# Kernel tuning notes

Measured on AMD Instinct MI355X. Metric: run time of the kernel, lower is better.

## Reference

```python
import jax, jax.numpy as jnp
import numpy as np

EPS = 1e-5
NEG_SLOPE = 0.01  # torch F.leaky_relu default


def _batchnorm(h, gamma, beta):
    # BatchNorm1d in training mode: batch stats over node dim, biased variance
    mu = jnp.mean(h, axis=0)
    var = jnp.mean((h - mu) ** 2, axis=0)
    return gamma * (h - mu) * jax.lax.rsqrt(var + EPS) + beta


def setup_inputs() -> dict:
    N, E, H, ED = 16384, 524288, 128, 16
    key = jax.random.key(0)
    ks = jax.random.split(key, 12)
    s = 1.0 / np.sqrt(H)
    return {
        "x": jax.random.normal(ks[0], (N, H), jnp.float32),
        "edge_index": jax.random.randint(ks[1], (2, E), 0, N, jnp.int64),
        "edge_attr": jax.random.normal(ks[2], (E, ED), jnp.float32),
        "Wq": jax.random.normal(ks[3], (H, H), jnp.float32) * s,
        "bq": jnp.zeros((H,), jnp.float32),
        "Wk": jax.random.normal(ks[4], (H, H), jnp.float32) * s,
        "bk": jnp.zeros((H,), jnp.float32),
        "Wv": jax.random.normal(ks[5], (H, H), jnp.float32) * s,
        "bv": jnp.zeros((H,), jnp.float32),
        "We": jax.random.normal(ks[6], (ED, 1), jnp.float32) * (1.0 / np.sqrt(ED)),
        "be": jnp.zeros((1,), jnp.float32),
        "bn1_g": jnp.ones((H,), jnp.float32),
        "bn1_b": jnp.zeros((H,), jnp.float32),
        "W1": jax.random.normal(ks[7], (H, 2 * H), jnp.float32) * s,
        "b1": jnp.zeros((2 * H,), jnp.float32),
        "W2": jax.random.normal(ks[8], (2 * H, H), jnp.float32) * (1.0 / np.sqrt(2 * H)),
        "b2": jnp.zeros((H,), jnp.float32),
        "bn2_g": jnp.ones((H,), jnp.float32),
        "bn2_b": jnp.zeros((H,), jnp.float32),
    }


def reference(x, edge_index, edge_attr, Wq, bq, Wk, bk, Wv, bv, We, be,
              bn1_g, bn1_b, W1, b1, W2, b2, bn2_g, bn2_b):
    N = x.shape[0]
    Q = x @ Wq + bq  # [N, H]
    K = x @ Wk + bk
    V = x @ Wv + bv
    Ebias = (edge_attr @ We + be)[:, 0]  # [E], num_heads == 1
    src, dst = edge_index[0], edge_index[1]
    # per-edge dot product over the FULL hidden dim (as in the source)
    scores = jnp.sum(Q[src] * K[dst], axis=1) + Ebias  # [E]
    scores = jnp.where(scores >= 0, scores, NEG_SLOPE * scores)
    # to_dense_adj scatter-adds edge_attr into a dense [N, N] adjacency
    adj = jnp.zeros((N, N), x.dtype).at[src, dst].add(scores)
    attn = jax.nn.softmax(adj, axis=1)  # dense softmax incl. zero non-edges
    x_new = attn @ V  # [N, H]
    h = _batchnorm(x + x_new, bn1_g, bn1_b)
    ffn = jax.nn.relu(h @ W1 + b1) @ W2 + b2
    return _batchnorm(h + ffn, bn2_g, bn2_b)
```

## Files before the change

kernel.cpp:

```cpp
#include <hip/hip_runtime.h>
#include <hip/hip_bf16.h>
#include <math.h>

#define H 128
#define H2 256
#define SLAB 96
#define LDA 136
#define LDA2 264
#define EPS 1e-5f

typedef __attribute__((ext_vector_type(8))) short s16x8;
typedef __attribute__((ext_vector_type(4))) float f32x4;

__device__ __forceinline__ unsigned short f2bf(float f) {
  unsigned u = __float_as_uint(f);
  unsigned r = (u + 0x7FFFu + ((u >> 16) & 1u)) >> 16;
  return (unsigned short)r;
}
__device__ __forceinline__ float bf2f(unsigned short s) {
  return __uint_as_float(((unsigned)s) << 16);
}

__global__ void wprep(const float* __restrict__ Wq, const float* __restrict__ Wk,
                      const float* __restrict__ Wv, const float* __restrict__ W1,
                      const float* __restrict__ W2,
                      short* qh, short* ql, short* kh, short* kl,
                      short* vh, short* w1h, short* w2h,
                      int* __restrict__ cnt, float* __restrict__ stats, int N)
{
  int job = blockIdx.z;
  if (job == 5) {
    int t = blockIdx.x * 256 + threadIdx.x;
    if (t < N) cnt[t] = 0;
    if (t < 72 * H) stats[t] = 0.f;
    return;
  }
  const float* src; short* dh; short* dl = nullptr; int Kd, Nn;
  if (job == 0)      { src = Wq; dh = qh;  dl = ql; Kd = 128; Nn = 128; }
  else if (job == 1) { src = Wk; dh = kh;  dl = kl; Kd = 128; Nn = 128; }
  else if (job == 2) { src = Wv; dh = vh;           Kd = 128; Nn = 128; }
  else if (job == 3) { src = W1; dh = w1h;          Kd = 128; Nn = 256; }
  else               { src = W2; dh = w2h;          Kd = 256; Nn = 128; }
  int t = blockIdx.x * 256 + threadIdx.x;
  if (t >= Kd * Nn) return;
  int n = t / Kd, k = t - n * Kd;
  float v = src[(size_t)k * Nn + n];
  unsigned short h = f2bf(v);
  dh[t] = (short)h;
  if (dl) dl[t] = (short)f2bf(v - bf2f(h));
}

__global__ __launch_bounds__(256) void qkv_mfma(
    const float* __restrict__ x,
    const short* __restrict__ Wqh, const short* __restrict__ Wql,
    const short* __restrict__ Wkh, const short* __restrict__ Wkl,
    const short* __restrict__ Wvh,
    const float* __restrict__ bq, const float* __restrict__ bk,
    const float* __restrict__ bv,
    float* __restrict__ Q, unsigned short* __restrict__ Kbf,
    unsigned short* __restrict__ Vbf, float* __restrict__ SVp)
{
  __shared__ __align__(16) short Ahi[64 * LDA];
  __shared__ __align__(16) short Alo[64 * LDA];
  int tid = threadIdx.x;
  int bm = blockIdx.x * 64;
  int wave = tid >> 6, lane = tid & 63;
  int quad = lane >> 4, l16 = lane & 15;
  int wn = wave * 32;

#pragma unroll
  for (int i = 0; i < 4; ++i) {
    int g = i * 256 + tid;
    int row = g >> 4, f = g & 15;
    const float4* xp = (const float4*)&x[(size_t)(bm + row) * H + f * 8];
    float4 v0 = xp[0], v1 = xp[1];
    float vv[8] = {v0.x, v0.y, v0.z, v0.w, v1.x, v1.y, v1.z, v1.w};
    s16x8 hv, lv;
#pragma unroll
    for (int j = 0; j < 8; ++j) {
      unsigned short hh = f2bf(vv[j]);
      hv[j] = (short)hh;
      lv[j] = (short)f2bf(vv[j] - bf2f(hh));
    }
    *(s16x8*)&Ahi[row * LDA + f * 8] = hv;
    *(s16x8*)&Alo[row * LDA + f * 8] = lv;
  }
  __syncthreads();

  for (int ph = 0; ph < 3; ++ph) {
    const short* Bh = (ph == 0) ? Wqh : (ph == 1) ? Wkh : Wvh;
    const short* Bl = (ph == 0) ? Wql : (ph == 1) ? Wkl : nullptr;

    s16x8 bh[2][4], bl2[2][4];
#pragma unroll
    for (int nt = 0; nt < 2; ++nt)
#pragma unroll
      for (int ks = 0; ks < 4; ++ks)
        bh[nt][ks] = *(const s16x8*)&Bh[(size_t)(wn + nt * 16 + l16) * H + ks * 32 + quad * 8];
    if (Bl) {
#pragma unroll
      for (int nt = 0; nt < 2; ++nt)
#pragma unroll
        for (int ks = 0; ks < 4; ++ks)
          bl2[nt][ks] = *(const s16x8*)&Bl[(size_t)(wn + nt * 16 + l16) * H + ks * 32 + quad * 8];
    }

    f32x4 acc[4][2];
#pragma unroll
    for (int mt = 0; mt < 4; ++mt)
#pragma unroll
      for (int nt = 0; nt < 2; ++nt) acc[mt][nt] = (f32x4){0.f, 0.f, 0.f, 0.f};

#pragma unroll
    for (int ks = 0; ks < 4; ++ks) {
      int kof = ks * 32 + quad * 8;
      s16x8 ah[4], al[4];
#pragma unroll
      for (int mt = 0; mt < 4; ++mt) {
        ah[mt] = *(s16x8*)&Ahi[(mt * 16 + l16) * LDA + kof];
        al[mt] = *(s16x8*)&Alo[(mt * 16 + l16) * LDA + kof];
      }
#pragma unroll
      for (int mt = 0; mt < 4; ++mt)
#pragma unroll
        for (int nt = 0; nt < 2; ++nt) {
          acc[mt][nt] = __builtin_amdgcn_mfma_f32_16x16x32_bf16(ah[mt], bh[nt][ks], acc[mt][nt], 0, 0, 0);
          if (ph < 2) {
            acc[mt][nt] = __builtin_amdgcn_mfma_f32_16x16x32_bf16(ah[mt], bl2[nt][ks], acc[mt][nt], 0, 0, 0);
            acc[mt][nt] = __builtin_amdgcn_mfma_f32_16x16x32_bf16(al[mt], bh[nt][ks], acc[mt][nt], 0, 0, 0);
          }
        }
    }

    if (ph == 0) {
#pragma unroll
      for (int nt = 0; nt < 2; ++nt) {
        int col = wn + nt * 16 + l16;
        float bb = bq[col];
#pragma unroll
        for (int mt = 0; mt < 4; ++mt)
#pragma unroll
          for (int r = 0; r < 4; ++r) {
            int row = bm + mt * 16 + quad * 4 + r;
            Q[(size_t)row * H + col] = acc[mt][nt][r] + bb;
          }
      }
    } else if (ph == 1) {
#pragma unroll
      for (int nt = 0; nt < 2; ++nt) {
        int col = wn + nt * 16 + l16;
        float bb = bk[col];
#pragma unroll
        for (int mt = 0; mt < 4; ++mt)
#pragma unroll
          for (int r = 0; r < 4; ++r) {
            int row = bm + mt * 16 + quad * 4 + r;
            Kbf[(size_t)row * H + col] = f2bf(acc[mt][nt][r] + bb);
          }
      }
    } else {
      int bank = blockIdx.x & 7;
#pragma unroll
      for (int nt = 0; nt < 2; ++nt) {
        int col = wn + nt * 16 + l16;
        float bb = bv[col];
        float ps = 0.f;
#pragma unroll
        for (int mt = 0; mt < 4; ++mt)
#pragma unroll
          for (int r = 0; r < 4; ++r) {
            int row = bm + mt * 16 + quad * 4 + r;
            float v = acc[mt][nt][r] + bb;
            Vbf[(size_t)row * H + col] = f2bf(v);
            ps += v;
          }
        ps += __shfl_xor(ps, 16);
        ps += __shfl_xor(ps, 32);
        if (quad == 0) atomicAdd(&SVp[bank * H + col], ps);
      }
    }
  }
}

__global__ void ebfill(const float* __restrict__ ea,
                       const float* __restrict__ We,
                       const float* __restrict__ be,
                       const int* __restrict__ ei,
                       int* __restrict__ cnt,
                       int2* __restrict__ slabDE, int E, int N)
{
  int grp = blockIdx.x & 7;
  int blk = blockIdx.x >> 3;
  int lo = grp * (N >> 3), hi = lo + (N >> 3);
  int per = E >> 8;
  int base = blk * per;
  float4 w0 = *(const float4*)&We[0], w1 = *(const float4*)&We[4];
  float4 w2 = *(const float4*)&We[8], w3 = *(const float4*)&We[12];
  float bias = be[0];
  for (int i = 0; i < per; i += 256) {
    int e = base + i + threadIdx.x;
    if (e >= E) continue;
    int src = ei[e];
    if (src < lo || src >= hi) continue;
    int dst = ei[E + e];
    const float4* p = (const float4*)&ea[(size_t)e * 16];
    float4 a0 = p[0], a1 = p[1], a2 = p[2], a3 = p[3];
    float s = a0.x * w0.x + a0.y * w0.y + a0.z * w0.z + a0.w * w0.w
            + a1.x * w1.x + a1.y * w1.y + a1.z * w1.z + a1.w * w1.w
            + a2.x * w2.x + a2.y * w2.y + a2.z * w2.z + a2.w * w2.w
            + a3.x * w3.x + a3.y * w3.y + a3.z * w3.z + a3.w * w3.w;
    s += bias;
    int pos = atomicAdd(&cnt[src], 1);
    if (pos < SLAB) {
      int2 rec; rec.x = dst; rec.y = __float_as_int(s);
      slabDE[src * SLAB + pos] = rec;
    }
  }
}

__global__ __launch_bounds__(256) void attn_fused(
    const float* __restrict__ x, const float* __restrict__ Q,
    const unsigned short* __restrict__ Kbf, const unsigned short* __restrict__ Vbf,
    const float* __restrict__ SVp, const int* __restrict__ cnt,
    const int2* __restrict__ slabDE,
    float* __restrict__ h1, float* __restrict__ sum1p, float* __restrict__ sq1p,
    int N)
{
  __shared__ float sv[8][SLAB];
  __shared__ int sd[8][SLAB];
  __shared__ unsigned char sown[8][SLAB];
  __shared__ float csum[H], csq[H], svf[H];
  int tid = threadIdx.x;
  int team = tid >> 5, lane = tid & 31;
  int i = blockIdx.x * 8 + team;
  int k = cnt[i]; if (k > SLAB) k = SLAB;
  int base = i * SLAB;

  if (tid < H) {
    csum[tid] = 0.f; csq[tid] = 0.f;
    float s = 0.f;
#pragma unroll
    for (int b = 0; b < 8; ++b) s += SVp[b * H + tid];
    svf[tid] = s;
  }

  for (int p = lane; p < k; p += 32) {
    int2 de = slabDE[base + p];
    sd[team][p] = de.x;
    sv[team][p] = __int_as_float(de.y);
  }
  __syncthreads();

  int sub8 = lane & 7, sub4 = lane >> 3;
  const float4* q4 = (const float4*)(Q + (size_t)i * H);
  float4 qa0 = q4[2 * sub8], qa1 = q4[2 * sub8 + 1];
  float4 qb0 = q4[16 + 2 * sub8], qb1 = q4[17 + 2 * sub8];
  for (int p0 = sub4 * 2; p0 < k; p0 += 8) {
    int d0 = sd[team][p0];
    bool has1 = (p0 + 1 < k);
    int d1 = has1 ? sd[team][p0 + 1] : d0;
    const s16x8* k0 = (const s16x8*)(Kbf + (size_t)d0 * H);
    const s16x8* k1 = (const s16x8*)(Kbf + (size_t)d1 * H);
    s16x8 ka0 = k0[sub8], kb0 = k0[8 + sub8];
    s16x8 ka1 = k1[sub8], kb1 = k1[8 + sub8];
    float p0_, p1_;
    p0_ = qa0.x * bf2f((unsigned short)ka0[0]) + qa0.y * bf2f((unsigned short)ka0[1])
        + qa0.z * bf2f((unsigned short)ka0[2]) + qa0.w * bf2f((unsigned short)ka0[3])
        + qa1.x * bf2f((unsigned short)ka0[4]) + qa1.y * bf2f((unsigned short)ka0[5])
        + qa1.z * bf2f((unsigned short)ka0[6]) + qa1.w * bf2f((unsigned short)ka0[7])
        + qb0.x * bf2f((unsigned short)kb0[0]) + qb0.y * bf2f((unsigned short)kb0[1])
        + qb0.z * bf2f((unsigned short)kb0[2]) + qb0.w * bf2f((unsigned short)kb0[3])
        + qb1.x * bf2f((unsigned short)kb0[4]) + qb1.y * bf2f((unsigned short)kb0[5])
        + qb1.z * bf2f((unsigned short)kb0[6]) + qb1.w * bf2f((unsigned short)kb0[7]);
    p1_ = qa0.x * bf2f((unsigned short)ka1[0]) + qa0.y * bf2f((unsigned short)ka1[1])
        + qa0.z * bf2f((unsigned short)ka1[2]) + qa0.w * bf2f((unsigned short)ka1[3])
        + qa1.x * bf2f((unsigned short)ka1[4]) + qa1.y * bf2f((unsigned short)ka1[5])
        + qa1.z * bf2f((unsigned short)ka1[6]) + qa1.w * bf2f((unsigned short)ka1[7])
        + qb0.x * bf2f((unsigned short)kb1[0]) + qb0.y * bf2f((unsigned short)kb1[1])
        + qb0.z * bf2f((unsigned short)kb1[2]) + qb0.w * bf2f((unsigned short)kb1[3])
        + qb1.x * bf2f((unsigned short)kb1[4]) + qb1.y * bf2f((unsigned short)kb1[5])
        + qb1.z * bf2f((unsigned short)kb1[6]) + qb1.w * bf2f((unsigned short)kb1[7]);
    p0_ += __shfl_xor(p0_, 1); p1_ += __shfl_xor(p1_, 1);
    p0_ += __shfl_xor(p0_, 2); p1_ += __shfl_xor(p1_, 2);
    p0_ += __shfl_xor(p0_, 4); p1_ += __shfl_xor(p1_, 4);
    if (sub8 == 0) {
      float s0 = p0_ + sv[team][p0];
      sv[team][p0] = (s0 >= 0.f) ? s0 : 0.01f * s0;
      if (has1) {
        float s1 = p1_ + sv[team][p0 + 1];
        sv[team][p0 + 1] = (s1 >= 0.f) ? s1 : 0.01f * s1;
      }
    }
  }

  for (int p = lane; p < k; p += 32) {
    int d = sd[team][p], o = p;
    for (int q = 0; q < p; ++q)
      if (sd[team][q] == d) { o = q; break; }
    sown[team][p] = (unsigned char)o;
  }
  for (int p = lane; p < k; p += 32)
    if (sown[team][p] != (unsigned char)p)
      atomicAdd(&sv[team][sown[team][p]], sv[team][p]);

  float m = 0.f;
  for (int p = lane; p < k; p += 32)
    if (sown[team][p] == (unsigned char)p) m = fmaxf(m, sv[team][p]);
#pragma unroll
  for (int mask = 16; mask; mask >>= 1) m = fmaxf(m, __shfl_xor(m, mask));
  float em = expf(-m);

  float zl = 0.f;
  for (int p = lane; p < k; p += 32) {
    float cf = 0.f;
    if (sown[team][p] == (unsigned char)p) cf = expf(sv[team][p] - m) - em;
    sv[team][p] = cf;
    zl += cf;
  }
#pragma unroll
  for (int mask = 16; mask; mask >>= 1) zl += __shfl_xor(zl, mask);
  float Zi = 1.f / ((float)N * em + zl);

  const ushort4* V4 = (const ushort4*)Vbf;
  float4 s4 = *(const float4*)&svf[lane * 4];
  float ax = em * s4.x, ay = em * s4.y, az = em * s4.z, aw = em * s4.w;
  int c = 0;
  for (; c + 8 <= k; c += 8) {
    float cf[8]; int dd[8]; ushort4 vv[8];
#pragma unroll
    for (int u = 0; u < 8; ++u) { cf[u] = sv[team][c + u]; dd[u] = sd[team][c + u]; }
#pragma unroll
    for (int u = 0; u < 8; ++u) vv[u] = V4[(size_t)dd[u] * 32 + lane];
#pragma unroll
    for (int u = 0; u < 8; ++u) {
      ax += cf[u] * bf2f(vv[u].x);
      ay += cf[u] * bf2f(vv[u].y);
      az += cf[u] * bf2f(vv[u].z);
      aw += cf[u] * bf2f(vv[u].w);
    }
  }
  for (; c < k; ++c) {
    float cf = sv[team][c];
    ushort4 v0 = V4[(size_t)sd[team][c] * 32 + lane];
    ax += cf * bf2f(v0.x); ay += cf * bf2f(v0.y);
    az += cf * bf2f(v0.z); aw += cf * bf2f(v0.w);
  }
  float4 xx = *(const float4*)&x[(size_t)i * H + lane * 4];
  float4 out;
  out.x = xx.x + ax * Zi; out.y = xx.y + ay * Zi;
  out.z = xx.z + az * Zi; out.w = xx.w + aw * Zi;
  *(float4*)&h1[(size_t)i * H + lane * 4] = out;

  int c0 = lane * 4;
  atomicAdd(&csum[c0 + 0], out.x); atomicAdd(&csq[c0 + 0], out.x * out.x);
  atomicAdd(&csum[c0 + 1], out.y); atomicAdd(&csq[c0 + 1], out.y * out.y);
  atomicAdd(&csum[c0 + 2], out.z); atomicAdd(&csq[c0 + 2], out.z * out.z);
  atomicAdd(&csum[c0 + 3], out.w); atomicAdd(&csq[c0 + 3], out.w * out.w);
  __syncthreads();
  if (tid < H) {
    int bank = blockIdx.x & 15;
    atomicAdd(&sum1p[bank * H + tid], csum[tid]);
    atomicAdd(&sq1p[bank * H + tid], csq[tid]);
  }
}

__global__ __launch_bounds__(256) void ffn_fused(
    const float* __restrict__ h1, const short* __restrict__ W1h,
    const float* __restrict__ b1, const short* __restrict__ W2h,
    const float* __restrict__ b2,
    const float* __restrict__ sum1p, const float* __restrict__ sq1p,
    const float* __restrict__ g1, const float* __restrict__ bb1,
    float* __restrict__ h2, float* __restrict__ sum2p, float* __restrict__ sq2p,
    float invN)
{
  __shared__ __align__(16) short As[32 * LDA];
  __shared__ __align__(16) short Ts[32 * LDA2];
  __shared__ float aF[H], bF[H];
  int tid = threadIdx.x;
  int bm = blockIdx.x * 32;
  int wave = tid >> 6, lane = tid & 63;
  int quad = lane >> 4, l16 = lane & 15;

  if (tid < H) {
    float s = 0.f, q = 0.f;
#pragma unroll
    for (int b = 0; b < 16; ++b) { s += sum1p[b * H + tid]; q += sq1p[b * H + tid]; }
    float mu = s * invN;
    float var = q * invN - mu * mu;
    float rs = rsqrtf(var + EPS);
    float a = g1[tid] * rs;
    aF[tid] = a;
    bF[tid] = bb1[tid] - a * mu;
  }
  __syncthreads();

  int f = tid & 15;
#pragma unroll
  for (int i = 0; i < 2; ++i) {
    int g = i * 256 + tid;
    int row = g >> 4;
    const float4* xp = (const float4*)&h1[(size_t)(bm + row) * H + f * 8];
    float4 v0 = xp[0], v1 = xp[1];
    float vv[8] = {v0.x, v0.y, v0.z, v0.w, v1.x, v1.y, v1.z, v1.w};
    s16x8 hv;
#pragma unroll
    for (int j = 0; j < 8; ++j) {
      int c = f * 8 + j;
      hv[j] = (short)f2bf(aF[c] * vv[j] + bF[c]);
    }
    *(s16x8*)&As[row * LDA + f * 8] = hv;
  }

  int wn1 = wave * 64;
  s16x8 b1f[4][4];
#pragma unroll
  for (int nt = 0; nt < 4; ++nt)
#pragma unroll
    for (int ks = 0; ks < 4; ++ks)
      b1f[nt][ks] = *(const s16x8*)&W1h[(size_t)(wn1 + nt * 16 + l16) * H + ks * 32 + quad * 8];
  __syncthreads();

  f32x4 acc1[2][4];
#pragma unroll
  for (int mt = 0; mt < 2; ++mt)
#pragma unroll
    for (int nt = 0; nt < 4; ++nt) acc1[mt][nt] = (f32x4){0.f, 0.f, 0.f, 0.f};

#pragma unroll
  for (int ks = 0; ks < 4; ++ks) {
    int kof = ks * 32 + quad * 8;
    s16x8 ah[2];
#pragma unroll
    for (int mt = 0; mt < 2; ++mt) ah[mt] = *(s16x8*)&As[(mt * 16 + l16) * LDA + kof];
#pragma unroll
    for (int mt = 0; mt < 2; ++mt)
#pragma unroll
      for (int nt = 0; nt < 4; ++nt)
        acc1[mt][nt] = __builtin_amdgcn_mfma_f32_16x16x32_bf16(ah[mt], b1f[nt][ks], acc1[mt][nt], 0, 0, 0);
  }

#pragma unroll
  for (int nt = 0; nt < 4; ++nt) {
    int col = wn1 + nt * 16 + l16;
    float bb = b1[col];
#pragma unroll
    for (int mt = 0; mt < 2; ++mt)
#pragma unroll
      for (int r = 0; r < 4; ++r) {
        int row = mt * 16 + quad * 4 + r;
        float v = acc1[mt][nt][r] + bb;
        v = v > 0.f ? v : 0.f;
        Ts[row * LDA2 + col] = (short)f2bf(v);
      }
  }

  int wn2 = wave * 32;
  s16x8 b2f[2][8];
#pragma unroll
  for (int nt = 0; nt < 2; ++nt)
#pragma unroll
    for (int ks = 0; ks < 8; ++ks)
      b2f[nt][ks] = *(const s16x8*)&W2h[(size_t)(wn2 + nt * 16 + l16) * H2 + ks * 32 + quad * 8];
  __syncthreads();

  f32x4 acc2[2][2];
#pragma unroll
  for (int mt = 0; mt < 2; ++mt)
#pragma unroll
    for (int nt = 0; nt < 2; ++nt) acc2[mt][nt] = (f32x4){0.f, 0.f, 0.f, 0.f};

#pragma unroll
  for (int ks = 0; ks < 8; ++ks) {
    int kof = ks * 32 + quad * 8;
    s16x8 ah[2];
#pragma unroll
    for (int mt = 0; mt < 2; ++mt) ah[mt] = *(s16x8*)&Ts[(mt * 16 + l16) * LDA2 + kof];
#pragma unroll
    for (int mt = 0; mt < 2; ++mt)
#pragma unroll
      for (int nt = 0; nt < 2; ++nt)
        acc2[mt][nt] = __builtin_amdgcn_mfma_f32_16x16x32_bf16(ah[mt], b2f[nt][ks], acc2[mt][nt], 0, 0, 0);
  }

  int bank = blockIdx.x & 15;
#pragma unroll
  for (int nt = 0; nt < 2; ++nt) {
    int col = wn2 + nt * 16 + l16;
    float ra = aF[col], rb = bF[col];
    float bb = b2[col];
    float ps = 0.f, pq = 0.f;
#pragma unroll
    for (int mt = 0; mt < 2; ++mt)
#pragma unroll
      for (int r = 0; r < 4; ++r) {
        int row = bm + mt * 16 + quad * 4 + r;
        float rr = ra * h1[(size_t)row * H + col] + rb;
        float v = acc2[mt][nt][r] + bb + rr;
        h2[(size_t)row * H + col] = v;
        ps += v; pq += v * v;
      }
    ps += __shfl_xor(ps, 16); ps += __shfl_xor(ps, 32);
    pq += __shfl_xor(pq, 16); pq += __shfl_xor(pq, 32);
    if (quad == 0) {
      atomicAdd(&sum2p[bank * H + col], ps);
      atomicAdd(&sq2p[bank * H + col], pq);
    }
  }
}

__global__ __launch_bounds__(256) void bn_apply(
    const float* __restrict__ X,
    const float* __restrict__ sum2p, const float* __restrict__ sq2p,
    const float* __restrict__ g2, const float* __restrict__ bb2,
    float* __restrict__ Y, size_t n4, float invN)
{
  __shared__ float A2s[H], B2s[H];
  int tid = threadIdx.x;
  if (tid < H) {
    float s = 0.f, q = 0.f;
#pragma unroll
    for (int b = 0; b < 16; ++b) { s += sum2p[b * H + tid]; q += sq2p[b * H + tid]; }
    float mu = s * invN;
    float var = q * invN - mu * mu;
    float rs = rsqrtf(var + EPS);
    float a = g2[tid] * rs;
    A2s[tid] = a;
    B2s[tid] = bb2[tid] - a * mu;
  }
  __syncthreads();
  size_t i = (size_t)blockIdx.x * blockDim.x + tid;
  if (i >= n4) return;
  float4 v = ((const float4*)X)[i];
  int c = (int)((i * 4) & (H - 1));
  float4 a = *(const float4*)&A2s[c];
  float4 b = *(const float4*)&B2s[c];
  v.x = a.x * v.x + b.x; v.y = a.y * v.y + b.y;
  v.z = a.z * v.z + b.z; v.w = a.w * v.w + b.w;
  ((float4*)Y)[i] = v;
}

extern "C" void kernel_launch(void* const* d_in, const int* in_sizes, int n_in,
                              void* d_out, int out_size, void* d_ws, size_t ws_size,
                              hipStream_t stream)
{
  const float* x  = (const float*)d_in[0];
  const int*   ei = (const int*)d_in[1];
  const float* ea = (const float*)d_in[2];
  const float* Wq = (const float*)d_in[3];
  const float* bq = (const float*)d_in[4];
  const float* Wk = (const float*)d_in[5];
  const float* bk = (const float*)d_in[6];
  const float* Wv = (const float*)d_in[7];
  const float* bv = (const float*)d_in[8];
  const float* We = (const float*)d_in[9];
  const float* be = (const float*)d_in[10];
  const float* g1 = (const float*)d_in[11];
  const float* bb1 = (const float*)d_in[12];
  const float* W1 = (const float*)d_in[13];
  const float* b1 = (const float*)d_in[14];
  const float* W2 = (const float*)d_in[15];
  const float* b2 = (const float*)d_in[16];
  const float* g2 = (const float*)d_in[17];
  const float* bb2 = (const float*)d_in[18];

  int N = in_sizes[0] / H;
  int E = in_sizes[2] / 16;
  size_t NH = (size_t)N * H;
  float invN = 1.0f / (float)N;

  float* Q   = (float*)d_ws;
  float* KmSlot = Q + NH;
  float* h1  = KmSlot + NH;
  unsigned short* Vbf = (unsigned short*)(h1 + NH);
  int2*  slabDE = (int2*)(Vbf + NH);
  int*   cnt    = (int*)(slabDE + (size_t)N * SLAB);
  float* stats  = (float*)(cnt + N);
  float* SVp   = stats;
  float* sum1p = stats + 8 * H;
  float* sq1p  = sum1p + 16 * H;
  float* sum2p = sq1p + 16 * H;
  float* sq2p  = sum2p + 16 * H;
  float* statsEnd = sq2p + 16 * H;
  short* wbuf = (short*)statsEnd;
  short* Wqh = wbuf;
  short* Wql = Wqh + 16384;
  short* Wkh = Wql + 16384;
  short* Wkl = Wkh + 16384;
  short* Wvh = Wkl + 16384;
  short* W1h = Wvh + 16384;
  short* W2h = W1h + 32768;
  unsigned short* Kbf = (unsigned short*)KmSlot;
  float* h2 = KmSlot;

  wprep<<<dim3(128, 1, 6), 256, 0, stream>>>(Wq, Wk, Wv, W1, W2,
      Wqh, Wql, Wkh, Wkl, Wvh, W1h, W2h, cnt, stats, N);

  qkv_mfma<<<dim3(N / 64), 256, 0, stream>>>(
      x, Wqh, Wql, Wkh, Wkl, Wvh, bq, bk, bv, Q, Kbf, Vbf, SVp);

  ebfill<<<dim3(2048), 256, 0, stream>>>(ea, We, be, ei, cnt, slabDE, E, N);

  attn_fused<<<dim3(N / 8), 256, 0, stream>>>(x, Q, Kbf, Vbf, SVp, cnt, slabDE,
                                              h1, sum1p, sq1p, N);

  ffn_fused<<<dim3(N / 32), 256, 0, stream>>>(h1, W1h, b1, W2h, b2,
      sum1p, sq1p, g1, bb1, h2, sum2p, sq2p, invN);

  bn_apply<<<dim3((int)((NH / 4 + 255) / 256)), 256, 0, stream>>>(
      h2, sum2p, sq2p, g2, bb2, (float*)d_out, NH / 4, invN);
}
```

Before: 222.0 us.

## Move edge score dot product into ebfill and store Q/K/V as fp16

Computes the per-edge Q·K score and leaky-relu inside the edge-fill kernel, using a shared-memory compaction of edges whose source falls in the block's node range. Each thread now does a full 128-wide fp16 dot product per edge, so the attention kernel no longer needs the score pass. Q, K and V are stored as fp16 instead of fp32/bf16, which halves Q traffic and changes precision. The cost is one thread reading 256B of Q and K serially per edge, which gives less coalesced access than the old 8-lane cooperative loads.

```diff
diff --git a/kernel.cpp b/kernel.cpp
--- a/kernel.cpp
+++ b/kernel.cpp
@@ -19,6 +19,12 @@
 }
 __device__ __forceinline__ float bf2f(unsigned short s) {
   return __uint_as_float(((unsigned)s) << 16);
+}
+__device__ __forceinline__ unsigned short f2h(float f) {
+  union { unsigned short s; _Float16 h; } c; c.h = (_Float16)f; return c.s;
+}
+__device__ __forceinline__ float h2f(unsigned short u) {
+  union { unsigned short s; _Float16 h; } c; c.s = u; return (float)c.h;
 }
 
 __global__ void wprep(const float* __restrict__ Wq, const float* __restrict__ Wk,
@@ -57,8 +63,8 @@
     const short* __restrict__ Wvh,
     const float* __restrict__ bq, const float* __restrict__ bk,
     const float* __restrict__ bv,
-    float* __restrict__ Q, unsigned short* __restrict__ Kbf,
-    unsigned short* __restrict__ Vbf, float* __restrict__ SVp)
+    unsigned short* __restrict__ Qh, unsigned short* __restrict__ Kh,
+    unsigned short* __restrict__ Vh, float* __restrict__ SVp)
 {
   __shared__ __align__(16) short Ahi[64 * LDA];
   __shared__ __align__(16) short Alo[64 * LDA];
@@ -142,7 +148,7 @@
 #pragma unroll
           for (int r = 0; r < 4; ++r) {
             int row = bm + mt * 16 + quad * 4 + r;
-            Q[(size_t)row * H + col] = acc[mt][nt][r] + bb;
+            Qh[(size_t)row * H + col] = f2h(acc[mt][nt][r] + bb);
           }
       }
     } else if (ph == 1) {
@@ -155,7 +161,7 @@
 #pragma unroll
           for (int r = 0; r < 4; ++r) {
             int row = bm + mt * 16 + quad * 4 + r;
-            Kbf[(size_t)row * H + col] = f2bf(acc[mt][nt][r] + bb);
+            Kh[(size_t)row * H + col] = f2h(acc[mt][nt][r] + bb);
           }
       }
     } else {
@@ -171,7 +177,7 @@
           for (int r = 0; r < 4; ++r) {
             int row = bm + mt * 16 + quad * 4 + r;
             float v = acc[mt][nt][r] + bb;
-            Vbf[(size_t)row * H + col] = f2bf(v);
+            Vh[(size_t)row * H + col] = f2h(v);
             ps += v;
           }
         ps += __shfl_xor(ps, 16);
@@ -182,13 +188,19 @@
   }
 }
 
-__global__ void ebfill(const float* __restrict__ ea,
-                       const float* __restrict__ We,
-                       const float* __restrict__ be,
-                       const int* __restrict__ ei,
-                       int* __restrict__ cnt,
-                       int2* __restrict__ slabDE, int E, int N)
+__global__ __launch_bounds__(256) void ebfill(
+    const float* __restrict__ ea,
+    const float* __restrict__ We,
+    const float* __restrict__ be,
+    const int* __restrict__ ei,
+    const unsigned short* __restrict__ Qh,
+    const unsigned short* __restrict__ Kh,
+    int* __restrict__ cnt,
+    int2* __restrict__ slabDE, int E, int N)
 {
+  __shared__ int qe[2048];
+  __shared__ int qn;
+  int tid = threadIdx.x;
   int grp = blockIdx.x & 7;
   int blk = blockIdx.x >> 3;
   int lo = grp * (N >> 3), hi = lo + (N >> 3);
@@ -197,11 +209,25 @@
   float4 w0 = *(const float4*)&We[0], w1 = *(const float4*)&We[4];
   float4 w2 = *(const float4*)&We[8], w3 = *(const float4*)&We[12];
   float bias = be[0];
+
+  if (tid == 0) qn = 0;
+  __syncthreads();
+
   for (int i = 0; i < per; i += 256) {
-    int e = base + i + threadIdx.x;
+    int e = base + i + tid;
     if (e >= E) continue;
     int src = ei[e];
-    if (src < lo || src >= hi) continue;
+    if (src >= lo && src < hi) {
+      int p = atomicAdd(&qn, 1);
+      qe[p] = e;
+    }
+  }
+  __syncthreads();
+
+  int m = qn;
+  for (int j = tid; j < m; j += 256) {
+    int e = qe[j];
+    int src = ei[e];
     int dst = ei[E + e];
     const float4* p = (const float4*)&ea[(size_t)e * 16];
     float4 a0 = p[0], a1 = p[1], a2 = p[2], a3 = p[3];
@@ -210,6 +236,25 @@
             + a2.x * w2.x + a2.y * w2.y + a2.z * w2.z + a2.w * w2.w
             + a3.x * w3.x + a3.y * w3.y + a3.z * w3.z + a3.w * w3.w;
     s += bias;
+
+    const s16x8* qp = (const s16x8*)(Qh + (size_t)src * H);
+    const s16x8* kp = (const s16x8*)(Kh + (size_t)dst * H);
+    float d0 = 0.f, d1 = 0.f, d2 = 0.f, d3 = 0.f;
+#pragma unroll 8
+    for (int c2 = 0; c2 < 16; ++c2) {
+      s16x8 qv = qp[c2], kv = kp[c2];
+      d0 += h2f((unsigned short)qv[0]) * h2f((unsigned short)kv[0]);
+      d1 += h2f((unsigned short)qv[1]) * h2f((unsigned short)kv[1]);
+      d2 += h2f((unsigned short)qv[2]) * h2f((unsigned short)kv[2]);
+      d3 += h2f((unsigned short)qv[3]) * h2f((unsigned short)kv[3]);
+      d0 += h2f((unsigned short)qv[4]) * h2f((unsigned short)kv[4]);
+      d1 += h2f((unsigned short)qv[5]) * h2f((unsigned short)kv[5]);
+      d2 += h2f((unsigned short)qv[6]) * h2f((unsigned short)kv[6]);
+      d3 += h2f((unsigned short)qv[7]) * h2f((unsigned short)kv[7]);
+    }
+    s += (d0 + d1) + (d2 + d3);
+    s = (s >= 0.f) ? s : 0.01f * s;
+
     int pos = atomicAdd(&cnt[src], 1);
     if (pos < SLAB) {
       int2 rec; rec.x = dst; rec.y = __float_as_int(s);
@@ -219,8 +264,8 @@
 }
 
 __global__ __launch_bounds__(256) void attn_fused(
-    const float* __restrict__ x, const float* __restrict__ Q,
-    const unsigned short* __restrict__ Kbf, const unsigned short* __restrict__ Vbf,
+    const float* __restrict__ x,
+    const unsigned short* __restrict__ Vh,
     const float* __restrict__ SVp, const int* __restrict__ cnt,
     const int2* __restrict__ slabDE,
     float* __restrict__ h1, float* __restrict__ sum1p, float* __restrict__ sq1p,
@@ -251,48 +296,6 @@
   }
   __syncthreads();
 
-  int sub8 = lane & 7, sub4 = lane >> 3;
-  const float4* q4 = (const float4*)(Q + (size_t)i * H);
-  float4 qa0 = q4[2 * sub8], qa1 = q4[2 * sub8 + 1];
-  float4 qb0 = q4[16 + 2 * sub8], qb1 = q4[17 + 2 * sub8];
-  for (int p0 = sub4 * 2; p0 < k; p0 += 8) {
-    int d0 = sd[team][p0];
-    bool has1 = (p0 + 1 < k);
-    int d1 = has1 ? sd[team][p0 + 1] : d0;
-    const s16x8* k0 = (const s16x8*)(Kbf + (size_t)d0 * H);
-    const s16x8* k1 = (const s16x8*)(Kbf + (size_t)d1 * H);
-    s16x8 ka0 = k0[sub8], kb0 = k0[8 + sub8];
-    s16x8 ka1 = k1[sub8], kb1 = k1[8 + sub8];
-    float p0_, p1_;
-    p0_ = qa0.x * bf2f((unsigned short)ka0[0]) + qa0.y * bf2f((unsigned short)ka0[1])
-        + qa0.z * bf2f((unsigned short)ka0[2]) + qa0.w * bf2f((unsigned short)ka0[3])
-        + qa1.x * bf2f((unsigned short)ka0[4]) + qa1.y * bf2f((unsigned short)ka0[5])
-        + qa1.z * bf2f((unsigned short)ka0[6]) + qa1.w * bf2f((unsigned short)ka0[7])
-        + qb0.x * bf2f((unsigned short)kb0[0]) + qb0.y * bf2f((unsigned short)kb0[1])
-        + qb0.z * bf2f((unsigned short)kb0[2]) + qb0.w * bf2f((unsigned short)kb0[3])
-        + qb1.x * bf2f((unsigned short)kb0[4]) + qb1.y * bf2f((unsigned short)kb0[5])
-        + qb1.z * bf2f((unsigned short)kb0[6]) + qb1.w * bf2f((unsigned short)kb0[7]);
-    p1_ = qa0.x * bf2f((unsigned short)ka1[0]) + qa0.y * bf2f((unsigned short)ka1[1])
-        + qa0.z * bf2f((unsigned short)ka1[2]) + qa0.w * bf2f((unsigned short)ka1[3])
-        + qa1.x * bf2f((unsigned short)ka1[4]) + qa1.y * bf2f((unsigned short)ka1[5])
-        + qa1.z * bf2f((unsigned short)ka1[6]) + qa1.w * bf2f((unsigned short)ka1[7])
-        + qb0.x * bf2f((unsigned short)kb1[0]) + qb0.y * bf2f((unsigned short)kb1[1])
-        + qb0.z * bf2f((unsigned short)kb1[2]) + qb0.w * bf2f((unsigned short)kb1[3])
-        + qb1.x * bf2f((unsigned short)kb1[4]) + qb1.y * bf2f((unsigned short)kb1[5])
-        + qb1.z * bf2f((unsigned short)kb1[6]) + qb1.w * bf2f((unsigned short)kb1[7]);
-    p0_ += __shfl_xor(p0_, 1); p1_ += __shfl_xor(p1_, 1);
-    p0_ += __shfl_xor(p0_, 2); p1_ += __shfl_xor(p1_, 2);
-    p0_ += __shfl_xor(p0_, 4); p1_ += __shfl_xor(p1_, 4);
-    if (sub8 == 0) {
-      float s0 = p0_ + sv[team][p0];
-      sv[team][p0] = (s0 >= 0.f) ? s0 : 0.01f * s0;
-      if (has1) {
-        float s1 = p1_ + sv[team][p0 + 1];
-        sv[team][p0 + 1] = (s1 >= 0.f) ? s1 : 0.01f * s1;
-      }
-    }
-  }
-
   for (int p = lane; p < k; p += 32) {
     int d = sd[team][p], o = p;
     for (int q = 0; q < p; ++q)
@@ -321,7 +324,7 @@
   for (int mask = 16; mask; mask >>= 1) zl += __shfl_xor(zl, mask);
   float Zi = 1.f / ((float)N * em + zl);
 
-  const ushort4* V4 = (const ushort4*)Vbf;
+  const ushort4* V4 = (const ushort4*)Vh;
   float4 s4 = *(const float4*)&svf[lane * 4];
   float ax = em * s4.x, ay = em * s4.y, az = em * s4.z, aw = em * s4.w;
   int c = 0;
@@ -333,17 +336,17 @@
     for (int u = 0; u < 8; ++u) vv[u] = V4[(size_t)dd[u] * 32 + lane];
 #pragma unroll
     for (int u = 0; u < 8; ++u) {
-      ax += cf[u] * bf2f(vv[u].x);
-      ay += cf[u] * bf2f(vv[u].y);
-      az += cf[u] * bf2f(vv[u].z);
-      aw += cf[u] * bf2f(vv[u].w);
+      ax += cf[u] * h2f(vv[u].x);
+      ay += cf[u] * h2f(vv[u].y);
+      az += cf[u] * h2f(vv[u].z);
+      aw += cf[u] * h2f(vv[u].w);
     }
   }
   for (; c < k; ++c) {
     float cf = sv[team][c];
     ushort4 v0 = V4[(size_t)sd[team][c] * 32 + lane];
-    ax += cf * bf2f(v0.x); ay += cf * bf2f(v0.y);
-    az += cf * bf2f(v0.z); aw += cf * bf2f(v0.w);
+    ax += cf * h2f(v0.x); ay += cf * h2f(v0.y);
+    az += cf * h2f(v0.z); aw += cf * h2f(v0.w);
   }
   float4 xx = *(const float4*)&x[(size_t)i * H + lane * 4];
   float4 out;
@@ -568,11 +571,11 @@
   size_t NH = (size_t)N * H;
   float invN = 1.0f / (float)N;
 
-  float* Q   = (float*)d_ws;
-  float* KmSlot = Q + NH;
-  float* h1  = KmSlot + NH;
-  unsigned short* Vbf = (unsigned short*)(h1 + NH);
-  int2*  slabDE = (int2*)(Vbf + NH);
+  unsigned short* Qh = (unsigned short*)d_ws;
+  unsigned short* Kh = Qh + NH;
+  unsigned short* Vh = Kh + NH;
+  float* h1  = (float*)(Vh + NH);
+  int2*  slabDE = (int2*)(h1 + NH);
   int*   cnt    = (int*)(slabDE + (size_t)N * SLAB);
   float* stats  = (float*)(cnt + N);
   float* SVp   = stats;
@@ -589,18 +592,17 @@
   short* Wvh = Wkl + 16384;
   short* W1h = Wvh + 16384;
   short* W2h = W1h + 32768;
-  unsigned short* Kbf = (unsigned short*)KmSlot;
-  float* h2 = KmSlot;
+  float* h2 = (float*)Qh;
 
   wprep<<<dim3(128, 1, 6), 256, 0, stream>>>(Wq, Wk, Wv, W1, W2,
       Wqh, Wql, Wkh, Wkl, Wvh, W1h, W2h, cnt, stats, N);
 
   qkv_mfma<<<dim3(N / 64), 256, 0, stream>>>(
-      x, Wqh, Wql, Wkh, Wkl, Wvh, bq, bk, bv, Q, Kbf, Vbf, SVp);
-
-  ebfill<<<dim3(2048), 256, 0, stream>>>(ea, We, be, ei, cnt, slabDE, E, N);
-
-  attn_fused<<<dim3(N / 8), 256, 0, stream>>>(x, Q, Kbf, Vbf, SVp, cnt, slabDE,
+      x, Wqh, Wql, Wkh, Wkl, Wvh, bq, bk, bv, Qh, Kh, Vh, SVp);
+
+  ebfill<<<dim3(2048), 256, 0, stream>>>(ea, We, be, ei, Qh, Kh, cnt, slabDE, E, N);
+
+  attn_fused<<<dim3(N / 8), 256, 0, stream>>>(x, Vh, SVp, cnt, slabDE,
                                               h1, sum1p, sq1p, N);
 
   ffn_fused<<<dim3(N / 32), 256, 0, stream>>>(h1, W1h, b1, W2h, b2,
```

After: 281.0 us. 26.6% more time.
